# Optimization experiments

Hardware: AMD Instinct MI355X
Metric: run time of the kernel (lower is better)

## Reference

```python
import jax, jax.numpy as jnp
import numpy as np

P = 16        # patch_size
SP = 8        # shift_pixels = int(patch_size * shift_ratio)
EPS = 1e-5    # torch LayerNorm default eps


def _bilinear_shift(img, sx, sy):
    """Replicates F.grid_sample(bilinear, zeros padding, align_corners=False)
    with a pure translation grid: out[y, x] = img[y + sy, x + sx] (bilinear)."""
    B, C, H, W = img.shape
    ys = jnp.arange(H, dtype=img.dtype) + jnp.asarray(sy, img.dtype)
    xs = jnp.arange(W, dtype=img.dtype) + jnp.asarray(sx, img.dtype)
    y0 = jnp.floor(ys)
    x0 = jnp.floor(xs)
    wy = ys - y0  # [H]
    wx = xs - x0  # [W]

    def gather(iy, ix):
        valid = ((iy >= 0) & (iy < H))[:, None] & ((ix >= 0) & (ix < W))[None, :]
        iyc = jnp.clip(iy, 0, H - 1).astype(jnp.int32)
        ixc = jnp.clip(ix, 0, W - 1).astype(jnp.int32)
        v = img[:, :, iyc][:, :, :, ixc]  # [B, C, H, W]
        return v * valid.astype(img.dtype)

    w00 = (1 - wy)[:, None] * (1 - wx)[None, :]
    w01 = (1 - wy)[:, None] * wx[None, :]
    w10 = wy[:, None] * (1 - wx)[None, :]
    w11 = wy[:, None] * wx[None, :]
    return (w00 * gather(y0, x0) + w01 * gather(y0, x0 + 1)
            + w10 * gather(y0 + 1, x0) + w11 * gather(y0 + 1, x0 + 1))


def reference(x, ln_gamma, ln_beta, w, b):
    B, C, H, W = x.shape
    # Original bug: shift_y = (shift_x * 2 / W) * 2 / H, so the effective
    # vertical pixel shift is ty*H/2 = 2*SP/W (sign of shift_x; dy ignored).
    ty_pix = 2.0 * SP / W
    right_up = _bilinear_shift(x, +SP, +ty_pix)
    left_up = _bilinear_shift(x, -SP, -ty_pix)
    right_down = _bilinear_shift(x, +SP, +ty_pix)
    left_down = _bilinear_shift(x, -SP, -ty_pix)
    xc = jnp.concatenate([x, left_up, right_up, left_down, right_down], axis=1)  # [B, 5C, H, W]
    C5 = xc.shape[1]
    h, ww = H // P, W // P
    # Rearrange 'B C (p1 h) (p2 w) -> B (h w) (C p1 p2)'  (p1/p2 are OUTER factors)
    p = xc.reshape(B, C5, P, h, P, ww)
    p = p.transpose(0, 3, 5, 1, 2, 4).reshape(B, h * ww, C5 * P * P)  # [B, 196, 3840]
    # LayerNorm (biased variance, as in torch)
    mu = p.mean(axis=-1, keepdims=True)
    var = p.var(axis=-1, keepdims=True)
    p = (p - mu) * jax.lax.rsqrt(var + EPS) * ln_gamma + ln_beta
    # Linear
    return p @ w + b  # [B, 196, 768]


def setup_inputs() -> dict:
    key = jax.random.key(0)
    k1, k2 = jax.random.split(key)
    d_in = P * P * 5 * 3  # 3840
    d_model = 768
    return {
        "x": jax.random.normal(k1, (64, 3, 224, 224), dtype=jnp.float32),
        "ln_gamma": jnp.ones((d_in,), dtype=jnp.float32),
        "ln_beta": jnp.zeros((d_in,), dtype=jnp.float32),
        "w": jax.random.normal(k2, (d_in, d_model), dtype=jnp.float32) / np.sqrt(d_in),
        "b": jnp.zeros((d_model,), dtype=jnp.float32),
    }
```

## Files before the change

kernel.cpp:

```cpp
#include <hip/hip_runtime.h>


typedef short bf16x8 __attribute__((ext_vector_type(8)));
typedef unsigned short u16x8 __attribute__((ext_vector_type(8)));
typedef float f32x4 __attribute__((ext_vector_type(4)));

#define GLOBAL_AS __attribute__((address_space(1)))
#define LDS_AS __attribute__((address_space(3)))

__device__ __forceinline__ unsigned short f2bf(float f) {
  union { float f; unsigned int u; } v;
  v.f = f;
  unsigned int u = v.u;
  unsigned int r = (u + 0x7FFFu + ((u >> 16) & 1u)) >> 16;
  return (unsigned short)r;
}

__global__ __launch_bounds__(256) void spt_fold_w(
    const float* __restrict__ gamma, const float* __restrict__ beta,
    const float* __restrict__ w, unsigned short* __restrict__ w2t,
    float* __restrict__ Gp, float* __restrict__ Bp)
{
  __shared__ float tile[16][257];
  const int f2blk = blockIdx.x * 16;
  const int jblk  = blockIdx.y * 256;
  const int t = threadIdx.x;
  const int j = jblk + t;
  float gacc = 0.f, bacc = 0.f;
  #pragma unroll
  for (int i = 0; i < 16; ++i) {
    const int f2 = f2blk + i;
    const int g = f2 / 768;
    const int rem = f2 % 768;
    float v, bv;
    if (g == 0) {
      const int f = rem;
      const float wv = w[(size_t)f * 768 + j];
      v = gamma[f] * wv;
      bv = beta[f] * wv;
    } else if (g == 1) {
      const int fa = 768 + rem, fb = 2304 + rem;
      const float wa = w[(size_t)fa * 768 + j], wb = w[(size_t)fb * 768 + j];
      v = gamma[fa] * wa + gamma[fb] * wb;
      bv = beta[fa] * wa + beta[fb] * wb;
    } else {
      const int fa = 1536 + rem, fb = 3072 + rem;
      const float wa = w[(size_t)fa * 768 + j], wb = w[(size_t)fb * 768 + j];
      v = gamma[fa] * wa + gamma[fb] * wb;
      bv = beta[fa] * wa + beta[fb] * wb;
    }
    tile[i][t] = v;
    gacc += v;
    bacc += bv;
  }
  __syncthreads();
  u16x8 lo, hi;
  #pragma unroll
  for (int i = 0; i < 8; ++i) {
    lo[i] = f2bf(tile[i][t]);
    hi[i] = f2bf(tile[8 + i][t]);
  }
  unsigned short* dst = w2t + (size_t)j * 2304 + f2blk;
  *(u16x8*)dst = lo;
  *(u16x8*)(dst + 8) = hi;
  Gp[blockIdx.x * 768 + j] = gacc;
  Bp[blockIdx.x * 768 + j] = bacc;
}

__global__ __launch_bounds__(256) void spt_gb(
    const float* __restrict__ Gp, const float* __restrict__ Bp,
    const float* __restrict__ bvec, float* __restrict__ G, float* __restrict__ Bt)
{
  const int j = blockIdx.x * 256 + threadIdx.x;
  float g = 0.f, bb = 0.f;
  for (int i = 0; i < 144; ++i) {
    g += Gp[i * 768 + j];
    bb += Bp[i * 768 + j];
  }
  G[j] = g;
  Bt[j] = bb + bvec[j];
}

__global__ __launch_bounds__(512) void spt_pack(
    const float* __restrict__ x, unsigned short* __restrict__ V,
    float2* __restrict__ stats)
{
  __shared__ unsigned short slab[14 * 2312];
  __shared__ float sred[8][224];
  __shared__ float qred[8][224];
  const int bi = blockIdx.x;
  const int b = bi / 14, hi = bi % 14;
  const int t = threadIdx.x;
  const float TW = 16.0f / 224.0f;

  const int q = t % 56;
  const int grp = t / 56;
  const int x4 = q * 4;

  int sloff[4];
  {
    int wi = x4 % 14, p2 = x4 / 14;
    #pragma unroll
    for (int j = 0; j < 4; ++j) {
      sloff[j] = wi * 2312 + p2;
      if (++wi == 14) { wi = 0; ++p2; }
    }
  }

  if (grp < 8) {
    f32x4 sAcc = {0.f, 0.f, 0.f, 0.f}, qAcc = {0.f, 0.f, 0.f, 0.f};
    #pragma unroll
    for (int it = 0; it < 6; ++it) {
      const int cp = grp * 6 + it;
      const int c = cp >> 4, p1 = cp & 15;
      const int y = p1 * 14 + hi;
      const float* row = x + ((size_t)(b * 3 + c)) * 50176 + (size_t)y * 224;
      const f32x4 xv = *(const f32x4*)(row + x4);
      f32x4 ra = {0.f,0.f,0.f,0.f}, rb = {0.f,0.f,0.f,0.f};
      f32x4 la = {0.f,0.f,0.f,0.f}, lb = {0.f,0.f,0.f,0.f};
      if (q < 54) {
        ra = *(const f32x4*)(row + x4 + 8);
        if (y < 223) rb = *(const f32x4*)(row + x4 + 8 + 224);
      }
      if (q >= 2) {
        la = *(const f32x4*)(row + x4 - 8);
        if (y > 0) lb = *(const f32x4*)(row + x4 - 8 - 224);
      }
      const f32x4 rv = (1.0f - TW) * ra + TW * rb;
      const f32x4 lv = (1.0f - TW) * la + TW * lb;
      sAcc += xv + 2.0f * (lv + rv);
      qAcc += xv * xv + 2.0f * (lv * lv + rv * rv);
      const int kb = c * 256 + p1 * 16;
      #pragma unroll
      for (int j = 0; j < 4; ++j) {
        slab[sloff[j] + kb]        = f2bf(xv[j]);
        slab[sloff[j] + kb + 768]  = f2bf(lv[j]);
        slab[sloff[j] + kb + 1536] = f2bf(rv[j]);
      }
    }
    #pragma unroll
    for (int j = 0; j < 4; ++j) {
      sred[grp][x4 + j] = sAcc[j];
      qred[grp][x4 + j] = qAcc[j];
    }
  }
  __syncthreads();

  if (t < 224) {
    float ss = 0.f, qq = 0.f;
    #pragma unroll
    for (int g = 0; g < 8; ++g) { ss += sred[g][t]; qq += qred[g][t]; }
    sred[0][t] = ss;
    qred[0][t] = qq;
  }
  __syncthreads();

  const int tok0 = b * 196 + hi * 14;
  if (t < 14) {
    float S = 0.f, Q = 0.f;
    #pragma unroll
    for (int p = 0; p < 16; ++p) { S += sred[0][t + 14 * p]; Q += qred[0][t + 14 * p]; }
    const float mu = S / 3840.f;
    const float var = Q / 3840.f - mu * mu;
    const float r = rsqrtf(var + 1e-5f);
    stats[tok0 + t] = make_float2(r, -mu * r);
  }

  for (int i = t; i < 14 * 288; i += 512) {
    const int wi2 = i / 288, off = i % 288;
    *(u16x8*)&V[(size_t)(tok0 + wi2) * 2304 + off * 8] =
        *(const u16x8*)&slab[wi2 * 2312 + off * 8];
  }
}

__global__ __launch_bounds__(256, 2) void spt_gemm(
    const unsigned short* __restrict__ V, const unsigned short* __restrict__ w2t,
    const float2* __restrict__ stats, const float* __restrict__ G,
    const float* __restrict__ Bt, float* __restrict__ out)
{
  __shared__ unsigned short Alds[2][224 * 64];
  __shared__ unsigned short Blds[2][96 * 64];

  const int orig = blockIdx.x;
  const int wgid = (orig & 7) * 56 + (orig >> 3);
  const int m0 = (wgid >> 3) * 224;
  const int n0 = (wgid & 7) * 96;

  if (orig & 1)   asm volatile("s_sleep 13" ::: "memory");
  if (orig & 256) asm volatile("s_sleep 13" ::: "memory");

  const int t = threadIdx.x;
  const int w = t >> 6, l = t & 63;
  const int wr = w >> 1;
  const int wn = w & 1;

  f32x4 acc[7][3] = {};

#define STAGE(pb, kt)                                                          \
  {                                                                            \
    const int k0s = (kt) << 6;                                                 \
    _Pragma("unroll") for (int i = 0; i < 7; ++i) {                            \
      const int c = i * 256 + t;                                               \
      const int row = c >> 3;                                                  \
      const int srcel = (((c & 7) ^ (row & 7)) << 3);                          \
      const unsigned short* ga = V + (size_t)(m0 + row) * 2304 + k0s + srcel;  \
      __builtin_amdgcn_global_load_lds((const GLOBAL_AS unsigned int*)ga,      \
          (LDS_AS unsigned int*)&Alds[pb][i * 2048 + w * 512], 16, 0, 0);      \
    }                                                                          \
    _Pragma("unroll") for (int i = 0; i < 3; ++i) {                            \
      const int c = i * 256 + t;                                               \
      const int row = c >> 3;                                                  \
      const int srcel = (((c & 7) ^ (row & 7)) << 3);                          \
      const unsigned short* gb = w2t + (size_t)(n0 + row) * 2304 + k0s + srcel;\
      __builtin_amdgcn_global_load_lds((const GLOBAL_AS unsigned int*)gb,      \
          (LDS_AS unsigned int*)&Blds[pb][i * 2048 + w * 512], 16, 0, 0);      \
    }                                                                          \
  }

#define COMPUTE(pb)                                                            \
  {                                                                            \
    const int lane15 = l & 15;                                                 \
    const int kcol = (l >> 4) << 4;                                            \
    bf16x8 bF[2][3], aF[2][7];                                                 \
    _Pragma("unroll") for (int kk = 0; kk < 2; ++kk) {                         \
      const int kb = kk * 64 + kcol;                                           \
      _Pragma("unroll") for (int n = 0; n < 3; ++n) {                          \
        const int row = wn * 48 + n * 16 + lane15;                             \
        const int phys = row * 128 + (kb ^ ((row & 7) << 4));                  \
        bF[kk][n] = *(const bf16x8*)&Blds[pb][phys >> 1];                      \
      }                                                                        \
      _Pragma("unroll") for (int m = 0; m < 7; ++m) {                          \
        const int row = wr * 112 + m * 16 + lane15;                            \
        const int phys = row * 128 + (kb ^ ((row & 7) << 4));                  \
        aF[kk][m] = *(const bf16x8*)&Alds[pb][phys >> 1];                      \
      }                                                                        \
    }                                                                          \
    __builtin_amdgcn_s_setprio(1);                                             \
    _Pragma("unroll") for (int kk = 0; kk < 2; ++kk)                           \
      _Pragma("unroll") for (int m = 0; m < 7; ++m)                            \
        _Pragma("unroll") for (int n = 0; n < 3; ++n)                          \
          acc[m][n] = __builtin_amdgcn_mfma_f32_16x16x32_bf16(aF[kk][m],       \
                          bF[kk][n], acc[m][n], 0, 0, 0);                      \
    __builtin_amdgcn_s_setprio(0);                                             \
  }

  STAGE(0, 0);
  int pb = 0;
  for (int kt = 0; kt < 35; ++kt) {
    STAGE(pb ^ 1, kt + 1);
    asm volatile("s_waitcnt vmcnt(10)\n\ts_barrier" ::: "memory");
    COMPUTE(pb);
    asm volatile("s_barrier" ::: "memory");
    pb ^= 1;
  }
  asm volatile("s_waitcnt vmcnt(0)\n\ts_barrier" ::: "memory");
  COMPUTE(pb);

  const int lane15 = l & 15;
  const int lg = (l >> 4) * 4;
  #pragma unroll
  for (int m = 0; m < 7; ++m) {
    const int rowb = m0 + wr * 112 + m * 16 + lg;
    float2 st[4];
    #pragma unroll
    for (int r = 0; r < 4; ++r) st[r] = stats[rowb + r];
    #pragma unroll
    for (int n = 0; n < 3; ++n) {
      const int col = n0 + wn * 48 + n * 16 + lane15;
      const float Gc = G[col];
      const float Bc = Bt[col];
      #pragma unroll
      for (int r = 0; r < 4; ++r) {
        out[(size_t)(rowb + r) * 768 + col] = st[r].x * acc[m][n][r] + st[r].y * Gc + Bc;
      }
    }
  }
#undef STAGE
#undef COMPUTE
}

extern "C" void kernel_launch(void* const* d_in, const int* in_sizes, int n_in,
                              void* d_out, int out_size, void* d_ws, size_t ws_size,
                              hipStream_t stream) {
  const float* x     = (const float*)d_in[0];
  const float* gamma = (const float*)d_in[1];
  const float* beta  = (const float*)d_in[2];
  const float* w     = (const float*)d_in[3];
  const float* bvec  = (const float*)d_in[4];
  float* out = (float*)d_out;

  char* ws = (char*)d_ws;
  unsigned short* V   = (unsigned short*)(ws);
  unsigned short* w2t = (unsigned short*)(ws + 57802752);
  float2* stats       = (float2*)(ws + 61341696);
  float* G            = (float*)(ws + 61442048);
  float* Bt           = (float*)(ws + 61445120);
  float* Gp           = (float*)(ws + 61448192);
  float* Bp           = (float*)(ws + 61890560);

  spt_pack<<<896, 512, 0, stream>>>(x, V, stats);
  spt_fold_w<<<dim3(144, 3), 256, 0, stream>>>(gamma, beta, w, w2t, Gp, Bp);
  spt_gb<<<3, 256, 0, stream>>>(Gp, Bp, bvec, G, Bt);
  spt_gemm<<<448, 256, 0, stream>>>(V, w2t, stats, G, Bt, out);
}
```

Before: 98.69 us.

## Load GEMM B fragments directly into registers, bypassing LDS, and remap pack blocks

In the GEMM, the B (weight) tile no longer goes through LDS: each wave loads its bf16 B fragments straight from global memory into registers, double-buffered across two register sets, with the k-loop unrolled by two. This removes the B LDS traffic and halves the kernel's LDS footprint, which may allow more resident workgroups. The cost is redundant global loads of B across waves and extra register pressure. It also drops the s_sleep staggering and swizzles the block index in the pack kernel to spread work differently across XCDs.

```diff
diff --git a/kernel.cpp b/kernel.cpp
--- a/kernel.cpp
+++ b/kernel.cpp
@@ -88,7 +88,8 @@
   __shared__ unsigned short slab[14 * 2312];
   __shared__ float sred[8][224];
   __shared__ float qred[8][224];
-  const int bi = blockIdx.x;
+  const int orig = blockIdx.x;
+  const int bi = (orig & 7) * 112 + (orig >> 3);
   const int b = bi / 14, hi = bi % 14;
   const int t = threadIdx.x;
   const float TW = 16.0f / 224.0f;
@@ -179,22 +180,22 @@
     const float* __restrict__ Bt, float* __restrict__ out)
 {
   __shared__ unsigned short Alds[2][224 * 64];
-  __shared__ unsigned short Blds[2][96 * 64];
 
   const int orig = blockIdx.x;
   const int wgid = (orig & 7) * 56 + (orig >> 3);
   const int m0 = (wgid >> 3) * 224;
   const int n0 = (wgid & 7) * 96;
-
-  if (orig & 1)   asm volatile("s_sleep 13" ::: "memory");
-  if (orig & 256) asm volatile("s_sleep 13" ::: "memory");
-
   const int t = threadIdx.x;
   const int w = t >> 6, l = t & 63;
   const int wr = w >> 1;
   const int wn = w & 1;
 
   f32x4 acc[7][3] = {};
+
+  const unsigned short* gBF[3];
+  #pragma unroll
+  for (int n = 0; n < 3; ++n)
+    gBF[n] = w2t + (size_t)(n0 + wn * 48 + n * 16 + (l & 15)) * 2304 + ((l >> 4) << 3);
 
 #define STAGE(pb, kt)                                                          \
   {                                                                            \
@@ -207,28 +208,24 @@
       __builtin_amdgcn_global_load_lds((const GLOBAL_AS unsigned int*)ga,      \
           (LDS_AS unsigned int*)&Alds[pb][i * 2048 + w * 512], 16, 0, 0);      \
     }                                                                          \
-    _Pragma("unroll") for (int i = 0; i < 3; ++i) {                            \
-      const int c = i * 256 + t;                                               \
-      const int row = c >> 3;                                                  \
-      const int srcel = (((c & 7) ^ (row & 7)) << 3);                          \
-      const unsigned short* gb = w2t + (size_t)(n0 + row) * 2304 + k0s + srcel;\
-      __builtin_amdgcn_global_load_lds((const GLOBAL_AS unsigned int*)gb,      \
-          (LDS_AS unsigned int*)&Blds[pb][i * 2048 + w * 512], 16, 0, 0);      \
+  }
+
+#define BLOAD(BF, kt)                                                          \
+  {                                                                            \
+    const int koff = (kt) << 6;                                                \
+    _Pragma("unroll") for (int n = 0; n < 3; ++n) {                            \
+      BF##0[n] = *(const bf16x8*)(gBF[n] + koff);                              \
+      BF##1[n] = *(const bf16x8*)(gBF[n] + koff + 32);                         \
     }                                                                          \
   }
 
-#define COMPUTE(pb)                                                            \
+#define COMPUTE(pb, B0, B1)                                                    \
   {                                                                            \
     const int lane15 = l & 15;                                                 \
     const int kcol = (l >> 4) << 4;                                            \
-    bf16x8 bF[2][3], aF[2][7];                                                 \
+    bf16x8 aF[2][7];                                                           \
     _Pragma("unroll") for (int kk = 0; kk < 2; ++kk) {                         \
       const int kb = kk * 64 + kcol;                                           \
-      _Pragma("unroll") for (int n = 0; n < 3; ++n) {                          \
-        const int row = wn * 48 + n * 16 + lane15;                             \
-        const int phys = row * 128 + (kb ^ ((row & 7) << 4));                  \
-        bF[kk][n] = *(const bf16x8*)&Blds[pb][phys >> 1];                      \
-      }                                                                        \
       _Pragma("unroll") for (int m = 0; m < 7; ++m) {                          \
         const int row = wr * 112 + m * 16 + lane15;                            \
         const int phys = row * 128 + (kb ^ ((row & 7) << 4));                  \
@@ -236,25 +233,41 @@
       }                                                                        \
     }                                                                          \
     __builtin_amdgcn_s_setprio(1);                                             \
-    _Pragma("unroll") for (int kk = 0; kk < 2; ++kk)                           \
-      _Pragma("unroll") for (int m = 0; m < 7; ++m)                            \
-        _Pragma("unroll") for (int n = 0; n < 3; ++n)                          \
-          acc[m][n] = __builtin_amdgcn_mfma_f32_16x16x32_bf16(aF[kk][m],       \
-                          bF[kk][n], acc[m][n], 0, 0, 0);                      \
+    _Pragma("unroll") for (int m = 0; m < 7; ++m)                              \
+      _Pragma("unroll") for (int n = 0; n < 3; ++n)                            \
+        acc[m][n] = __builtin_amdgcn_mfma_f32_16x16x32_bf16(aF[0][m], B0[n],   \
+                                                            acc[m][n], 0, 0, 0); \
+    _Pragma("unroll") for (int m = 0; m < 7; ++m)                              \
+      _Pragma("unroll") for (int n = 0; n < 3; ++n)                            \
+        acc[m][n] = __builtin_amdgcn_mfma_f32_16x16x32_bf16(aF[1][m], B1[n],   \
+                                                            acc[m][n], 0, 0, 0); \
     __builtin_amdgcn_s_setprio(0);                                             \
   }
 
+  bf16x8 bX0[3], bX1[3], bY0[3], bY1[3];
+
   STAGE(0, 0);
-  int pb = 0;
-  for (int kt = 0; kt < 35; ++kt) {
-    STAGE(pb ^ 1, kt + 1);
-    asm volatile("s_waitcnt vmcnt(10)\n\ts_barrier" ::: "memory");
-    COMPUTE(pb);
+  BLOAD(bX, 0);
+  for (int i = 0; i < 17; ++i) {
+    const int kt = i * 2;
+    STAGE(1, kt + 1);
+    BLOAD(bY, kt + 1);
+    asm volatile("s_waitcnt vmcnt(13)\n\ts_barrier" ::: "memory");
+    COMPUTE(0, bX0, bX1);
     asm volatile("s_barrier" ::: "memory");
-    pb ^= 1;
-  }
+    STAGE(0, kt + 2);
+    BLOAD(bX, kt + 2);
+    asm volatile("s_waitcnt vmcnt(13)\n\ts_barrier" ::: "memory");
+    COMPUTE(1, bY0, bY1);
+    asm volatile("s_barrier" ::: "memory");
+  }
+  STAGE(1, 35);
+  BLOAD(bY, 35);
+  asm volatile("s_waitcnt vmcnt(13)\n\ts_barrier" ::: "memory");
+  COMPUTE(0, bX0, bX1);
+  asm volatile("s_barrier" ::: "memory");
   asm volatile("s_waitcnt vmcnt(0)\n\ts_barrier" ::: "memory");
-  COMPUTE(pb);
+  COMPUTE(1, bY0, bY1);
 
   const int lane15 = l & 15;
   const int lg = (l >> 4) * 4;
@@ -276,6 +289,7 @@
     }
   }
 #undef STAGE
+#undef BLOAD
 #undef COMPUTE
 }
 
```

Measured after the change: 117.1 us. +18.6%, slower.

## Restructure GEMM into 512-thread triple-buffered tiles with split A/B loader waves

Applied to the files above, without the earlier changes.

The GEMM now uses 224x192 tiles with 8 waves per block (224 blocks instead of 448), triple-buffered LDS, and a finely interleaved schedule. Half the waves stage A while the other half stage B, and the k-step is split into sub-phases with barriers between LDS reads and MFMA bursts. The pack kernel's block index is also remapped across XCDs. The aim is larger B reuse per block and better overlap of global loads with MFMA. The cost is one block per CU, many more barriers, and heavy LDS use.

```diff
diff --git a/kernel.cpp b/kernel.cpp
--- a/kernel.cpp
+++ b/kernel.cpp
@@ -88,7 +88,8 @@
   __shared__ unsigned short slab[14 * 2312];
   __shared__ float sred[8][224];
   __shared__ float qred[8][224];
-  const int bi = blockIdx.x;
+  const int orig = blockIdx.x;
+  const int bi = (orig & 7) * 112 + (orig >> 3);
   const int b = bi / 14, hi = bi % 14;
   const int t = threadIdx.x;
   const float TW = 16.0f / 224.0f;
@@ -173,90 +174,129 @@
   }
 }
 
-__global__ __launch_bounds__(256, 2) void spt_gemm(
+__global__ __launch_bounds__(512, 1) void spt_gemm(
     const unsigned short* __restrict__ V, const unsigned short* __restrict__ w2t,
     const float2* __restrict__ stats, const float* __restrict__ G,
     const float* __restrict__ Bt, float* __restrict__ out)
 {
-  __shared__ unsigned short Alds[2][224 * 64];
-  __shared__ unsigned short Blds[2][96 * 64];
+  __shared__ unsigned short Al[3][224 * 64];
+  __shared__ unsigned short Bl[3][192 * 64];
 
   const int orig = blockIdx.x;
-  const int wgid = (orig & 7) * 56 + (orig >> 3);
-  const int m0 = (wgid >> 3) * 224;
-  const int n0 = (wgid & 7) * 96;
-
-  if (orig & 1)   asm volatile("s_sleep 13" ::: "memory");
-  if (orig & 256) asm volatile("s_sleep 13" ::: "memory");
-
+  const int wgid = (orig & 7) * 28 + (orig >> 3);
+  const int m0 = (wgid >> 2) * 224;
+  const int n0 = (wgid & 3) * 192;
   const int t = threadIdx.x;
   const int w = t >> 6, l = t & 63;
-  const int wr = w >> 1;
-  const int wn = w & 1;
+  const int wr = w >> 2;
+  const int wn = w & 3;
+  const bool isA = (w < 4);
+  const int ts = isA ? t : (t - 256);
 
   f32x4 acc[7][3] = {};
-
-#define STAGE(pb, kt)                                                          \
-  {                                                                            \
-    const int k0s = (kt) << 6;                                                 \
-    _Pragma("unroll") for (int i = 0; i < 7; ++i) {                            \
-      const int c = i * 256 + t;                                               \
-      const int row = c >> 3;                                                  \
-      const int srcel = (((c & 7) ^ (row & 7)) << 3);                          \
-      const unsigned short* ga = V + (size_t)(m0 + row) * 2304 + k0s + srcel;  \
-      __builtin_amdgcn_global_load_lds((const GLOBAL_AS unsigned int*)ga,      \
-          (LDS_AS unsigned int*)&Alds[pb][i * 2048 + w * 512], 16, 0, 0);      \
-    }                                                                          \
-    _Pragma("unroll") for (int i = 0; i < 3; ++i) {                            \
-      const int c = i * 256 + t;                                               \
-      const int row = c >> 3;                                                  \
-      const int srcel = (((c & 7) ^ (row & 7)) << 3);                          \
-      const unsigned short* gb = w2t + (size_t)(n0 + row) * 2304 + k0s + srcel;\
-      __builtin_amdgcn_global_load_lds((const GLOBAL_AS unsigned int*)gb,      \
-          (LDS_AS unsigned int*)&Blds[pb][i * 2048 + w * 512], 16, 0, 0);      \
-    }                                                                          \
-  }
-
-#define COMPUTE(pb)                                                            \
-  {                                                                            \
-    const int lane15 = l & 15;                                                 \
-    const int kcol = (l >> 4) << 4;                                            \
-    bf16x8 bF[2][3], aF[2][7];                                                 \
-    _Pragma("unroll") for (int kk = 0; kk < 2; ++kk) {                         \
-      const int kb = kk * 64 + kcol;                                           \
-      _Pragma("unroll") for (int n = 0; n < 3; ++n) {                          \
-        const int row = wn * 48 + n * 16 + lane15;                             \
-        const int phys = row * 128 + (kb ^ ((row & 7) << 4));                  \
-        bF[kk][n] = *(const bf16x8*)&Blds[pb][phys >> 1];                      \
-      }                                                                        \
-      _Pragma("unroll") for (int m = 0; m < 7; ++m) {                          \
-        const int row = wr * 112 + m * 16 + lane15;                            \
-        const int phys = row * 128 + (kb ^ ((row & 7) << 4));                  \
-        aF[kk][m] = *(const bf16x8*)&Alds[pb][phys >> 1];                      \
-      }                                                                        \
-    }                                                                          \
-    __builtin_amdgcn_s_setprio(1);                                             \
-    _Pragma("unroll") for (int kk = 0; kk < 2; ++kk)                           \
-      _Pragma("unroll") for (int m = 0; m < 7; ++m)                            \
-        _Pragma("unroll") for (int n = 0; n < 3; ++n)                          \
-          acc[m][n] = __builtin_amdgcn_mfma_f32_16x16x32_bf16(aF[kk][m],       \
-                          bF[kk][n], acc[m][n], 0, 0, 0);                      \
-    __builtin_amdgcn_s_setprio(0);                                             \
-  }
-
-  STAGE(0, 0);
-  int pb = 0;
-  for (int kt = 0; kt < 35; ++kt) {
-    STAGE(pb ^ 1, kt + 1);
-    asm volatile("s_waitcnt vmcnt(10)\n\ts_barrier" ::: "memory");
-    COMPUTE(pb);
-    asm volatile("s_barrier" ::: "memory");
-    pb ^= 1;
-  }
-  asm volatile("s_waitcnt vmcnt(0)\n\ts_barrier" ::: "memory");
-  COMPUTE(pb);
+  bf16x8 aF[4], aG[3], bF[3];
 
   const int lane15 = l & 15;
+  const int kcol = (l >> 4) << 4;
+  const int srow = ts >> 3;
+  const int srcel = (((ts & 7) ^ ((ts >> 3) & 7)) << 3);
+
+#define STG1(P, kt)                                                            \
+  if (isA) {                                                                   \
+    _Pragma("unroll") for (int i = 0; i < 4; ++i)                              \
+      __builtin_amdgcn_global_load_lds(                                        \
+        (const GLOBAL_AS unsigned int*)(V + (size_t)(m0 + i * 32 + srow) * 2304 + (kt) * 64 + srcel), \
+        (LDS_AS unsigned int*)&Al[P][(i * 256 + ts) * 8], 16, 0, 0);           \
+  } else {                                                                     \
+    _Pragma("unroll") for (int i = 0; i < 3; ++i)                              \
+      __builtin_amdgcn_global_load_lds(                                        \
+        (const GLOBAL_AS unsigned int*)(w2t + (size_t)(n0 + i * 32 + srow) * 2304 + (kt) * 64 + srcel), \
+        (LDS_AS unsigned int*)&Bl[P][(i * 256 + ts) * 8], 16, 0, 0);           \
+  }
+#define STG2(P, kt)                                                            \
+  if (isA) {                                                                   \
+    _Pragma("unroll") for (int i = 4; i < 7; ++i)                              \
+      __builtin_amdgcn_global_load_lds(                                        \
+        (const GLOBAL_AS unsigned int*)(V + (size_t)(m0 + i * 32 + srow) * 2304 + (kt) * 64 + srcel), \
+        (LDS_AS unsigned int*)&Al[P][(i * 256 + ts) * 8], 16, 0, 0);           \
+  } else {                                                                     \
+    _Pragma("unroll") for (int i = 3; i < 6; ++i)                              \
+      __builtin_amdgcn_global_load_lds(                                        \
+        (const GLOBAL_AS unsigned int*)(w2t + (size_t)(n0 + i * 32 + srow) * 2304 + (kt) * 64 + srcel), \
+        (LDS_AS unsigned int*)&Bl[P][(i * 256 + ts) * 8], 16, 0, 0);           \
+  }
+
+#define RA03(P, kh)                                                            \
+  _Pragma("unroll") for (int mi = 0; mi < 4; ++mi) {                           \
+    const int row = wr * 112 + mi * 16 + lane15;                               \
+    const int phys = row * 128 + (((kh) + kcol) ^ ((row & 7) << 4));           \
+    aF[mi] = *(const bf16x8*)&Al[P][phys >> 1];                                \
+  }
+#define RA46(P, kh)                                                            \
+  _Pragma("unroll") for (int mi = 0; mi < 3; ++mi) {                           \
+    const int row = wr * 112 + (mi + 4) * 16 + lane15;                         \
+    const int phys = row * 128 + (((kh) + kcol) ^ ((row & 7) << 4));           \
+    aG[mi] = *(const bf16x8*)&Al[P][phys >> 1];                                \
+  }
+#define RB(P, kh)                                                              \
+  _Pragma("unroll") for (int ni = 0; ni < 3; ++ni) {                           \
+    const int row = wn * 48 + ni * 16 + lane15;                                \
+    const int phys = row * 128 + (((kh) + kcol) ^ ((row & 7) << 4));           \
+    bF[ni] = *(const bf16x8*)&Bl[P][phys >> 1];                                \
+  }
+
+#define M03                                                                    \
+  _Pragma("unroll") for (int mi = 0; mi < 4; ++mi)                             \
+    _Pragma("unroll") for (int ni = 0; ni < 3; ++ni)                           \
+      acc[mi][ni] = __builtin_amdgcn_mfma_f32_16x16x32_bf16(aF[mi], bF[ni], acc[mi][ni], 0, 0, 0);
+#define M46                                                                    \
+  _Pragma("unroll") for (int mi = 0; mi < 3; ++mi)                             \
+    _Pragma("unroll") for (int ni = 0; ni < 3; ++ni)                           \
+      acc[mi + 4][ni] = __builtin_amdgcn_mfma_f32_16x16x32_bf16(aG[mi], bF[ni], acc[mi + 4][ni], 0, 0, 0);
+
+#define BARLG asm volatile("s_barrier\n\ts_waitcnt lgkmcnt(0)" ::: "memory")
+#define BARE  asm volatile("s_barrier" ::: "memory")
+#define PR1 __builtin_amdgcn_s_setprio(1)
+#define PR0 __builtin_amdgcn_s_setprio(0)
+#define VMC                                                                    \
+  if (isA) asm volatile("s_waitcnt vmcnt(7)" ::: "memory");                    \
+  else     asm volatile("s_waitcnt vmcnt(6)" ::: "memory");
+
+#define PAIR(bA, bB, bS2, bS3, t2, t3)                                         \
+  RA03(bA, 0);  RB(bA, 0);  STG1(bS2, t2); BARLG; PR1; M03; PR0; BARE;         \
+  RA46(bA, 0);              STG2(bS2, t2); BARLG; PR1; M46; PR0; BARE;         \
+  RA03(bA, 64); RB(bA, 64);                BARLG; PR1; M03; PR0; BARE;         \
+  RA46(bA, 64);             VMC;           BARLG; PR1; M46; PR0; BARE;         \
+  RA03(bB, 0);  RB(bB, 0);  STG1(bS3, t3); BARLG; PR1; M03; PR0; BARE;         \
+  RA46(bB, 0);              STG2(bS3, t3); BARLG; PR1; M46; PR0; BARE;         \
+  RA03(bB, 64); RB(bB, 64);                BARLG; PR1; M03; PR0; BARE;         \
+  RA46(bB, 64);             VMC;           BARLG; PR1; M46; PR0; BARE;
+
+  STG1(0, 0); STG2(0, 0);
+  STG1(1, 1); STG2(1, 1);
+  VMC;
+  BARE;
+
+  for (int i = 0; i < 5; ++i) {
+    const int b = 6 * i;
+    PAIR(0, 1, 2, 0, b + 2, b + 3)
+    PAIR(2, 0, 1, 2, b + 4, b + 5)
+    PAIR(1, 2, 0, 1, b + 6, b + 7)
+  }
+  PAIR(0, 1, 2, 0, 32, 33)
+  PAIR(2, 0, 1, 2, 34, 35)
+
+  RA03(1, 0);  RB(1, 0);  BARLG; PR1; M03; PR0; BARE;
+  RA46(1, 0);             BARLG; PR1; M46; PR0; BARE;
+  RA03(1, 64); RB(1, 64); BARLG; PR1; M03; PR0; BARE;
+  RA46(1, 64); asm volatile("s_waitcnt vmcnt(0)" ::: "memory");
+                          BARLG; PR1; M46; PR0; BARE;
+  RA03(2, 0);  RB(2, 0);  BARLG; PR1; M03; PR0; BARE;
+  RA46(2, 0);             BARLG; PR1; M46; PR0; BARE;
+  RA03(2, 64); RB(2, 64); BARLG; PR1; M03; PR0; BARE;
+  RA46(2, 64);            asm volatile("s_waitcnt lgkmcnt(0)" ::: "memory");
+                          PR1; M46; PR0;
+
   const int lg = (l >> 4) * 4;
   #pragma unroll
   for (int m = 0; m < 7; ++m) {
@@ -275,8 +315,19 @@
       }
     }
   }
-#undef STAGE
-#undef COMPUTE
+#undef STG1
+#undef STG2
+#undef RA03
+#undef RA46
+#undef RB
+#undef M03
+#undef M46
+#undef BARLG
+#undef BARE
+#undef PR1
+#undef PR0
+#undef VMC
+#undef PAIR
 }
 
 extern "C" void kernel_launch(void* const* d_in, const int* in_sizes, int n_in,
@@ -301,5 +352,5 @@
   spt_pack<<<896, 512, 0, stream>>>(x, V, stats);
   spt_fold_w<<<dim3(144, 3), 256, 0, stream>>>(gamma, beta, w, w2t, Gp, Bp);
   spt_gb<<<3, 256, 0, stream>>>(Gp, Bp, bvec, G, Bt);
-  spt_gemm<<<448, 256, 0, stream>>>(V, w2t, stats, G, Bt, out);
-}
+  spt_gemm<<<224, 512, 0, stream>>>(V, w2t, stats, G, Bt, out);
+}
```

Result: faster. 91.84 us (-6.9%).

## Merge pack and weight-fold kernels into one launch; remove GEMM sleep stagger

Applied to the files above, without the earlier changes.

Combines the activation packing kernel and the weight-folding kernel into a single launch. Block indices select which role a block plays, and the fold blocks now handle 32 rows with 512 threads. It also remaps pack block indices in an XCD-interleaved order and deletes the s_sleep staggering at the start of the GEMM. The intent is to cut one launch gap and let the two independent preprocessing tasks run concurrently on the GPU. The trade-off is that the fold blocks now reserve the larger shared-memory footprint, which may reduce their occupancy.

```diff
diff --git a/kernel.cpp b/kernel.cpp
--- a/kernel.cpp
+++ b/kernel.cpp
@@ -16,55 +16,153 @@
   return (unsigned short)r;
 }
 
-__global__ __launch_bounds__(256) void spt_fold_w(
-    const float* __restrict__ gamma, const float* __restrict__ beta,
-    const float* __restrict__ w, unsigned short* __restrict__ w2t,
-    float* __restrict__ Gp, float* __restrict__ Bp)
+__global__ __launch_bounds__(512) void spt_prep(
+    const float* __restrict__ x, const float* __restrict__ gamma,
+    const float* __restrict__ beta, const float* __restrict__ w,
+    unsigned short* __restrict__ V, float2* __restrict__ stats,
+    unsigned short* __restrict__ w2t, float* __restrict__ Gp,
+    float* __restrict__ Bp)
 {
-  __shared__ float tile[16][257];
-  const int f2blk = blockIdx.x * 16;
-  const int jblk  = blockIdx.y * 256;
+  __shared__ __align__(16) char smem[79072];
   const int t = threadIdx.x;
-  const int j = jblk + t;
-  float gacc = 0.f, bacc = 0.f;
-  #pragma unroll
-  for (int i = 0; i < 16; ++i) {
-    const int f2 = f2blk + i;
-    const int g = f2 / 768;
-    const int rem = f2 % 768;
-    float v, bv;
-    if (g == 0) {
-      const int f = rem;
-      const float wv = w[(size_t)f * 768 + j];
-      v = gamma[f] * wv;
-      bv = beta[f] * wv;
-    } else if (g == 1) {
-      const int fa = 768 + rem, fb = 2304 + rem;
-      const float wa = w[(size_t)fa * 768 + j], wb = w[(size_t)fb * 768 + j];
-      v = gamma[fa] * wa + gamma[fb] * wb;
-      bv = beta[fa] * wa + beta[fb] * wb;
-    } else {
-      const int fa = 1536 + rem, fb = 3072 + rem;
-      const float wa = w[(size_t)fa * 768 + j], wb = w[(size_t)fb * 768 + j];
-      v = gamma[fa] * wa + gamma[fb] * wb;
-      bv = beta[fa] * wa + beta[fb] * wb;
-    }
-    tile[i][t] = v;
-    gacc += v;
-    bacc += bv;
-  }
-  __syncthreads();
-  u16x8 lo, hi;
-  #pragma unroll
-  for (int i = 0; i < 8; ++i) {
-    lo[i] = f2bf(tile[i][t]);
-    hi[i] = f2bf(tile[8 + i][t]);
-  }
-  unsigned short* dst = w2t + (size_t)j * 2304 + f2blk;
-  *(u16x8*)dst = lo;
-  *(u16x8*)(dst + 8) = hi;
-  Gp[blockIdx.x * 768 + j] = gacc;
-  Bp[blockIdx.x * 768 + j] = bacc;
+
+  if (blockIdx.x < 896) {
+    unsigned short* slab = (unsigned short*)smem;
+    float* sred = (float*)(smem + 64736);
+    float* qred = sred + 8 * 224;
+    const int orig = blockIdx.x;
+    const int bi = (orig & 7) * 112 + (orig >> 3);
+    const int b = bi / 14, hi = bi % 14;
+    const float TW = 16.0f / 224.0f;
+
+    const int q = t % 56;
+    const int grp = t / 56;
+    const int x4 = q * 4;
+
+    int sloff[4];
+    {
+      int wi = x4 % 14, p2 = x4 / 14;
+      #pragma unroll
+      for (int j = 0; j < 4; ++j) {
+        sloff[j] = wi * 2312 + p2;
+        if (++wi == 14) { wi = 0; ++p2; }
+      }
+    }
+
+    if (grp < 8) {
+      f32x4 sAcc = {0.f, 0.f, 0.f, 0.f}, qAcc = {0.f, 0.f, 0.f, 0.f};
+      #pragma unroll
+      for (int it = 0; it < 6; ++it) {
+        const int cp = grp * 6 + it;
+        const int c = cp >> 4, p1 = cp & 15;
+        const int y = p1 * 14 + hi;
+        const float* row = x + ((size_t)(b * 3 + c)) * 50176 + (size_t)y * 224;
+        const f32x4 xv = *(const f32x4*)(row + x4);
+        f32x4 ra = {0.f,0.f,0.f,0.f}, rb = {0.f,0.f,0.f,0.f};
+        f32x4 la = {0.f,0.f,0.f,0.f}, lb = {0.f,0.f,0.f,0.f};
+        if (q < 54) {
+          ra = *(const f32x4*)(row + x4 + 8);
+          if (y < 223) rb = *(const f32x4*)(row + x4 + 8 + 224);
+        }
+        if (q >= 2) {
+          la = *(const f32x4*)(row + x4 - 8);
+          if (y > 0) lb = *(const f32x4*)(row + x4 - 8 - 224);
+        }
+        const f32x4 rv = (1.0f - TW) * ra + TW * rb;
+        const f32x4 lv = (1.0f - TW) * la + TW * lb;
+        sAcc += xv + 2.0f * (lv + rv);
+        qAcc += xv * xv + 2.0f * (lv * lv + rv * rv);
+        const int kb = c * 256 + p1 * 16;
+        #pragma unroll
+        for (int j = 0; j < 4; ++j) {
+          slab[sloff[j] + kb]        = f2bf(xv[j]);
+          slab[sloff[j] + kb + 768]  = f2bf(lv[j]);
+          slab[sloff[j] + kb + 1536] = f2bf(rv[j]);
+        }
+      }
+      #pragma unroll
+      for (int j = 0; j < 4; ++j) {
+        sred[grp * 224 + x4 + j] = sAcc[j];
+        qred[grp * 224 + x4 + j] = qAcc[j];
+      }
+    }
+    __syncthreads();
+
+    if (t < 224) {
+      float ss = 0.f, qq = 0.f;
+      #pragma unroll
+      for (int g = 0; g < 8; ++g) { ss += sred[g * 224 + t]; qq += qred[g * 224 + t]; }
+      sred[t] = ss;
+      qred[t] = qq;
+    }
+    __syncthreads();
+
+    const int tok0 = b * 196 + hi * 14;
+    if (t < 14) {
+      float S = 0.f, Q = 0.f;
+      #pragma unroll
+      for (int p = 0; p < 16; ++p) { S += sred[t + 14 * p]; Q += qred[t + 14 * p]; }
+      const float mu = S / 3840.f;
+      const float var = Q / 3840.f - mu * mu;
+      const float r = rsqrtf(var + 1e-5f);
+      stats[tok0 + t] = make_float2(r, -mu * r);
+    }
+
+    for (int i = t; i < 14 * 288; i += 512) {
+      const int wi2 = i / 288, off = i % 288;
+      *(u16x8*)&V[(size_t)(tok0 + wi2) * 2304 + off * 8] =
+          *(const u16x8*)&slab[wi2 * 2312 + off * 8];
+    }
+  } else {
+    float* tileF = (float*)smem;
+    const int bx = blockIdx.x - 896;
+    const int fx = bx / 3;
+    const int fy = bx % 3;
+    const int half = t >> 8;
+    const int tt = t & 255;
+    const int j = fy * 256 + tt;
+    const int f2blk = fx * 32 + half * 16;
+
+    float gacc = 0.f, bacc = 0.f;
+    #pragma unroll
+    for (int i = 0; i < 16; ++i) {
+      const int f2 = f2blk + i;
+      const int g = f2 / 768;
+      const int rem = f2 % 768;
+      float v, bv;
+      if (g == 0) {
+        const int f = rem;
+        const float wv = w[(size_t)f * 768 + j];
+        v = gamma[f] * wv;
+        bv = beta[f] * wv;
+      } else if (g == 1) {
+        const int fa = 768 + rem, fb = 2304 + rem;
+        const float wa = w[(size_t)fa * 768 + j], wb = w[(size_t)fb * 768 + j];
+        v = gamma[fa] * wa + gamma[fb] * wb;
+        bv = beta[fa] * wa + beta[fb] * wb;
+      } else {
+        const int fa = 1536 + rem, fb = 3072 + rem;
+        const float wa = w[(size_t)fa * 768 + j], wb = w[(size_t)fb * 768 + j];
+        v = gamma[fa] * wa + gamma[fb] * wb;
+        bv = beta[fa] * wa + beta[fb] * wb;
+      }
+      tileF[(half * 16 + i) * 257 + tt] = v;
+      gacc += v;
+      bacc += bv;
+    }
+    __syncthreads();
+    u16x8 lo, hi;
+    #pragma unroll
+    for (int i = 0; i < 8; ++i) {
+      lo[i] = f2bf(tileF[(half * 16 + i) * 257 + tt]);
+      hi[i] = f2bf(tileF[(half * 16 + 8 + i) * 257 + tt]);
+    }
+    unsigned short* dst = w2t + (size_t)j * 2304 + f2blk;
+    *(u16x8*)dst = lo;
+    *(u16x8*)(dst + 8) = hi;
+    Gp[(fx * 2 + half) * 768 + j] = gacc;
+    Bp[(fx * 2 + half) * 768 + j] = bacc;
+  }
 }
 
 __global__ __launch_bounds__(256) void spt_gb(
@@ -81,98 +179,6 @@
   Bt[j] = bb + bvec[j];
 }
 
-__global__ __launch_bounds__(512) void spt_pack(
-    const float* __restrict__ x, unsigned short* __restrict__ V,
-    float2* __restrict__ stats)
-{
-  __shared__ unsigned short slab[14 * 2312];
-  __shared__ float sred[8][224];
-  __shared__ float qred[8][224];
-  const int bi = blockIdx.x;
-  const int b = bi / 14, hi = bi % 14;
-  const int t = threadIdx.x;
-  const float TW = 16.0f / 224.0f;
-
-  const int q = t % 56;
-  const int grp = t / 56;
-  const int x4 = q * 4;
-
-  int sloff[4];
-  {
-    int wi = x4 % 14, p2 = x4 / 14;
-    #pragma unroll
-    for (int j = 0; j < 4; ++j) {
-      sloff[j] = wi * 2312 + p2;
-      if (++wi == 14) { wi = 0; ++p2; }
-    }
-  }
-
-  if (grp < 8) {
-    f32x4 sAcc = {0.f, 0.f, 0.f, 0.f}, qAcc = {0.f, 0.f, 0.f, 0.f};
-    #pragma unroll
-    for (int it = 0; it < 6; ++it) {
-      const int cp = grp * 6 + it;
-      const int c = cp >> 4, p1 = cp & 15;
-      const int y = p1 * 14 + hi;
-      const float* row = x + ((size_t)(b * 3 + c)) * 50176 + (size_t)y * 224;
-      const f32x4 xv = *(const f32x4*)(row + x4);
-      f32x4 ra = {0.f,0.f,0.f,0.f}, rb = {0.f,0.f,0.f,0.f};
-      f32x4 la = {0.f,0.f,0.f,0.f}, lb = {0.f,0.f,0.f,0.f};
-      if (q < 54) {
-        ra = *(const f32x4*)(row + x4 + 8);
-        if (y < 223) rb = *(const f32x4*)(row + x4 + 8 + 224);
-      }
-      if (q >= 2) {
-        la = *(const f32x4*)(row + x4 - 8);
-        if (y > 0) lb = *(const f32x4*)(row + x4 - 8 - 224);
-      }
-      const f32x4 rv = (1.0f - TW) * ra + TW * rb;
-      const f32x4 lv = (1.0f - TW) * la + TW * lb;
-      sAcc += xv + 2.0f * (lv + rv);
-      qAcc += xv * xv + 2.0f * (lv * lv + rv * rv);
-      const int kb = c * 256 + p1 * 16;
-      #pragma unroll
-      for (int j = 0; j < 4; ++j) {
-        slab[sloff[j] + kb]        = f2bf(xv[j]);
-        slab[sloff[j] + kb + 768]  = f2bf(lv[j]);
-        slab[sloff[j] + kb + 1536] = f2bf(rv[j]);
-      }
-    }
-    #pragma unroll
-    for (int j = 0; j < 4; ++j) {
-      sred[grp][x4 + j] = sAcc[j];
-      qred[grp][x4 + j] = qAcc[j];
-    }
-  }
-  __syncthreads();
-
-  if (t < 224) {
-    float ss = 0.f, qq = 0.f;
-    #pragma unroll
-    for (int g = 0; g < 8; ++g) { ss += sred[g][t]; qq += qred[g][t]; }
-    sred[0][t] = ss;
-    qred[0][t] = qq;
-  }
-  __syncthreads();
-
-  const int tok0 = b * 196 + hi * 14;
-  if (t < 14) {
-    float S = 0.f, Q = 0.f;
-    #pragma unroll
-    for (int p = 0; p < 16; ++p) { S += sred[0][t + 14 * p]; Q += qred[0][t + 14 * p]; }
-    const float mu = S / 3840.f;
-    const float var = Q / 3840.f - mu * mu;
-    const float r = rsqrtf(var + 1e-5f);
-    stats[tok0 + t] = make_float2(r, -mu * r);
-  }
-
-  for (int i = t; i < 14 * 288; i += 512) {
-    const int wi2 = i / 288, off = i % 288;
-    *(u16x8*)&V[(size_t)(tok0 + wi2) * 2304 + off * 8] =
-        *(const u16x8*)&slab[wi2 * 2312 + off * 8];
-  }
-}
-
 __global__ __launch_bounds__(256, 2) void spt_gemm(
     const unsigned short* __restrict__ V, const unsigned short* __restrict__ w2t,
     const float2* __restrict__ stats, const float* __restrict__ G,
@@ -185,10 +191,6 @@
   const int wgid = (orig & 7) * 56 + (orig >> 3);
   const int m0 = (wgid >> 3) * 224;
   const int n0 = (wgid & 7) * 96;
-
-  if (orig & 1)   asm volatile("s_sleep 13" ::: "memory");
-  if (orig & 256) asm volatile("s_sleep 13" ::: "memory");
-
   const int t = threadIdx.x;
   const int w = t >> 6, l = t & 63;
   const int wr = w >> 1;
@@ -298,8 +300,7 @@
   float* Gp           = (float*)(ws + 61448192);
   float* Bp           = (float*)(ws + 61890560);
 
-  spt_pack<<<896, 512, 0, stream>>>(x, V, stats);
-  spt_fold_w<<<dim3(144, 3), 256, 0, stream>>>(gamma, beta, w, w2t, Gp, Bp);
+  spt_prep<<<1112, 512, 0, stream>>>(x, gamma, beta, w, V, stats, w2t, Gp, Bp);
   spt_gb<<<3, 256, 0, stream>>>(Gp, Bp, bvec, G, Bt);
   spt_gemm<<<448, 256, 0, stream>>>(V, w2t, stats, G, Bt, out);
 }
```

Result: faster. 90.26 us (-8.5%).
